# Optimization experiments

Measured on AMD Instinct MI355X. Metric: run time of the kernel, lower is better.

The kernel has to match this reference:

```python
import jax, jax.numpy as jnp
import numpy as np

NUM_HEADS = 16
D_IN = 1024
D_OUT = 64  # = D_IN // NUM_HEADS
N = 2048


def setup_inputs() -> dict:
    key = jax.random.key(0)
    kx, kq, kk, kv, ko = jax.random.split(key, 5)
    x = jax.random.normal(kx, (N, D_IN), dtype=jnp.float32)
    # per-head projection weights, stacked over heads (torch code keeps a
    # Python list of SelfAttention modules; stacking is the vectorized form)
    q_proj = jax.random.normal(kq, (NUM_HEADS, D_IN, D_OUT), dtype=jnp.float32)
    k_proj = jax.random.normal(kk, (NUM_HEADS, D_IN, D_OUT), dtype=jnp.float32)
    v_proj = jax.random.normal(kv, (NUM_HEADS, D_IN, D_OUT), dtype=jnp.float32)
    o_proj = jax.random.normal(ko, (D_IN, D_IN), dtype=jnp.float32)
    return {"x": x, "q_proj": q_proj, "k_proj": k_proj, "v_proj": v_proj, "o_proj": o_proj}


def reference(x, q_proj, k_proj, v_proj, o_proj):
    d_out = q_proj.shape[-1]
    # per-head projections: [H, N, E]
    q = jnp.einsum('nd,hde->hne', x, q_proj)
    k = jnp.einsum('nd,hde->hne', x, k_proj)
    v = jnp.einsum('nd,hde->hne', x, v_proj)
    # full NxN scores per head (matches the naive torch implementation's math)
    scores = jnp.einsum('hne,hme->hnm', q, k) / jnp.sqrt(jnp.float32(d_out))
    attn = jax.nn.softmax(scores, axis=-1)
    ctx = jnp.einsum('hnm,hme->hne', attn, v)
    # concat heads along the feature dim (head 0 first, as in torch.cat)
    h, n, e = ctx.shape
    out = jnp.transpose(ctx, (1, 0, 2)).reshape(n, h * e)
    return out @ o_proj
```

## Files before the change

kernel.cpp:

```cpp
#include <hip/hip_runtime.h>

#define H 16
#define N 2048
#define E 64
#define D 1024

typedef __attribute__((ext_vector_type(8))) short bf16x8;
typedef __attribute__((ext_vector_type(4))) float f32x4;
typedef __attribute__((ext_vector_type(4))) unsigned int u32x4;

__device__ __forceinline__ float bf2f(unsigned short u) {
    union { unsigned int i; float f; } v;
    v.i = ((unsigned int)u) << 16;
    return v.f;
}
__device__ __forceinline__ unsigned short f2bf(float f) {
    unsigned int u = __float_as_uint(f);
    return (unsigned short)((u + 0x7fffu + ((u >> 16) & 1u)) >> 16);
}
__device__ __forceinline__ unsigned int cvtpk(float lo, float hi) {
    unsigned int r;
    asm("v_cvt_pk_bf16_f32 %0, %1, %2" : "=v"(r) : "v"(lo), "v"(hi));
    return r;
}
__device__ __forceinline__ bf16x8 pk4(unsigned int a, unsigned int b,
                                      unsigned int c, unsigned int d) {
    union { u32x4 u; bf16x8 h; } x;
    x.u = (u32x4){a, b, c, d};
    return x.h;
}
#define MFMA(a, b, c) __builtin_amdgcn_mfma_f32_16x16x32_bf16(a, b, c, 0, 0, 0)

typedef __attribute__((address_space(3))) unsigned int lds_u32;
typedef const __attribute__((address_space(1))) unsigned int glb_u32;
__device__ __forceinline__ void dma16(const unsigned short* g, unsigned short* l) {
    __builtin_amdgcn_global_load_lds((glb_u32*)g, (lds_u32*)l, 16, 0, 0);
}

__device__ __forceinline__ int sw8(int row, int c)  { return row * 64  + ((c ^ (row & 7)) << 3); }

__global__ __launch_bounds__(256) void convert_all_kernel(
    const float* __restrict__ x,
    const float* __restrict__ qw, const float* __restrict__ kw,
    const float* __restrict__ vw, const float* __restrict__ ow,
    unsigned short* __restrict__ xh, unsigned short* __restrict__ xl,
    unsigned short* __restrict__ wBh, unsigned short* __restrict__ wBl,
    unsigned short* __restrict__ wvt, unsigned short* __restrict__ woh)
{
    __shared__ float ts[64][65];
    const int b0 = blockIdx.x;
    const int t = threadIdx.x;
    if (b0 < 2048) {
        const int i = (b0 * 256 + t) * 4;
        const float4 v = *(const float4*)&x[i];
        ushort4 hh, ll;
        hh.x = f2bf(v.x); ll.x = f2bf(v.x - bf2f(hh.x));
        hh.y = f2bf(v.y); ll.y = f2bf(v.y - bf2f(hh.y));
        hh.z = f2bf(v.z); ll.z = f2bf(v.z - bf2f(hh.z));
        hh.w = f2bf(v.w); ll.w = f2bf(v.w - bf2f(hh.w));
        *(ushort4*)&xh[i] = hh;
        *(ushort4*)&xl[i] = ll;
        return;
    }
    const int b = b0 - 2048;
    const float* src;
    int rs, dt, orow0;
    bool has_lo;
    unsigned short *dh, *dl;
    if (b < 768) {
        const int which = b >> 8, r = b & 255, h = r >> 4;
        dt = r & 15;
        src = (which == 0 ? qw : which == 1 ? kw : vw) + ((size_t)h * D + dt * 64) * E;
        rs = E;
        if (which == 0)      { dh = wBh; dl = wBl; orow0 = h * 64;        has_lo = true; }
        else if (which == 1) { dh = wBh; dl = wBl; orow0 = 1024 + h * 64; has_lo = true; }
        else                 { dh = wvt; dl = wBl; orow0 = h * 64;        has_lo = false; }
    } else {
        const int r = b - 768, ct = r >> 4;
        dt = r & 15;
        src = ow + (size_t)(dt * 64) * D + ct * 64;
        rs = D;
        orow0 = ct * 64;
        dh = woh; dl = wBl; has_lo = false;
    }
    {
        const int row = t >> 2, cb = (t & 3) * 16;
        #pragma unroll
        for (int j = 0; j < 16; j += 4) {
            const float4 v = *(const float4*)&src[row * rs + cb + j];
            ts[row][cb + j + 0] = v.x;
            ts[row][cb + j + 1] = v.y;
            ts[row][cb + j + 2] = v.z;
            ts[row][cb + j + 3] = v.w;
        }
    }
    __syncthreads();
    {
        const int cl = t >> 2, dp = (t & 3) * 16;
        bf16x8 hv0, hv1, lv0, lv1;
        #pragma unroll
        for (int i = 0; i < 16; ++i) {
            const float f = ts[dp + i][cl];
            const unsigned short hh = f2bf(f);
            const unsigned short lo = f2bf(f - bf2f(hh));
            if (i < 8) { hv0[i] = (short)hh; lv0[i] = (short)lo; }
            else       { hv1[i - 8] = (short)hh; lv1[i - 8] = (short)lo; }
        }
        const size_t o = (size_t)(orow0 + cl) * D + dt * 64 + dp;
        *(bf16x8*)&dh[o] = hv0;
        *(bf16x8*)&dh[o + 8] = hv1;
        if (has_lo) {
            *(bf16x8*)&dl[o] = lv0;
            *(bf16x8*)&dl[o + 8] = lv1;
        }
    }
}

__global__ __launch_bounds__(256, 3) void qkv_kernel(
    const unsigned short* __restrict__ xh, const unsigned short* __restrict__ xl,
    const unsigned short* __restrict__ wBh, const unsigned short* __restrict__ wBl,
    const unsigned short* __restrict__ wvt,
    unsigned short* __restrict__ Qh, unsigned short* __restrict__ Ql,
    unsigned short* __restrict__ Kh, unsigned short* __restrict__ Kl,
    unsigned short* __restrict__ Vt)
{
    __shared__ unsigned short ash[128 * 64], asl[128 * 64];
    __shared__ unsigned short bsh[64 * 64], bsl[64 * 64];
    const int n0 = blockIdx.x * 128;
    const int ct0 = blockIdx.y;
    const int sec = ct0 >> 4;
    const int hh = ct0 & 15;
    const bool isv = (sec == 2);
    const unsigned short* Bh = isv ? wvt : wBh;
    const size_t brow0 = (sec == 1 ? 1024 : 0) + hh * 64;

    const int t = threadIdx.x;
    const int lane = t & 63, wvi = t >> 6, quad = lane >> 4, l15 = lane & 15;

    f32x4 acc[2][4];
    #pragma unroll
    for (int i = 0; i < 2; ++i)
        #pragma unroll
        for (int j = 0; j < 4; ++j) acc[i][j] = (f32x4){0.f, 0.f, 0.f, 0.f};

    for (int k0 = 0; k0 < D; k0 += 64) {
        __syncthreads();
        #pragma unroll
        for (int p = 0; p < 4; ++p) {
            const int row = p * 32 + wvi * 8 + (lane >> 3);
            const int lc = (lane & 7) ^ (row & 7);
            const int lo = p * 2048 + wvi * 512 + lane * 8;
            const size_t ga = (size_t)(n0 + row) * D + k0 + lc * 8;
            dma16(&xh[ga], &ash[lo]);
            if (!isv) dma16(&xl[ga], &asl[lo]);
        }
        #pragma unroll
        for (int p = 0; p < 2; ++p) {
            const int row = p * 32 + wvi * 8 + (lane >> 3);
            const int lc = (lane & 7) ^ (row & 7);
            const int lo = p * 2048 + wvi * 512 + lane * 8;
            const size_t gb = (brow0 + row) * D + k0 + lc * 8;
            dma16(&Bh[gb], &bsh[lo]);
            if (!isv) dma16(&wBl[gb], &bsl[lo]);
        }
        __syncthreads();

        #pragma unroll
        for (int kwi = 0; kwi < 2; ++kwi) {
            const int c = kwi * 4 + quad;
            bf16x8 ah[2], al[2], bh[4], bl[4];
            #pragma unroll
            for (int i = 0; i < 2; ++i) {
                ah[i] = *(const bf16x8*)&ash[sw8(wvi * 32 + i * 16 + l15, c)];
                if (!isv) al[i] = *(const bf16x8*)&asl[sw8(wvi * 32 + i * 16 + l15, c)];
            }
            #pragma unroll
            for (int j = 0; j < 4; ++j) {
                bh[j] = *(const bf16x8*)&bsh[sw8(j * 16 + l15, c)];
                if (!isv) bl[j] = *(const bf16x8*)&bsl[sw8(j * 16 + l15, c)];
            }
            #pragma unroll
            for (int i = 0; i < 2; ++i)
                #pragma unroll
                for (int j = 0; j < 4; ++j) {
                    acc[i][j] = MFMA(ah[i], bh[j], acc[i][j]);
                    if (!isv) {
                        acc[i][j] = MFMA(ah[i], bl[j], acc[i][j]);
                        acc[i][j] = MFMA(al[i], bh[j], acc[i][j]);
                    }
                }
        }
    }

    if (isv) {
        #pragma unroll
        for (int j = 0; j < 4; ++j) {
            const int e = j * 16 + l15;
            #pragma unroll
            for (int i = 0; i < 2; ++i) {
                const int nb = n0 + wvi * 32 + i * 16 + quad * 4;
                ushort4 pk;
                pk.x = f2bf(acc[i][j][0]);
                pk.y = f2bf(acc[i][j][1]);
                pk.z = f2bf(acc[i][j][2]);
                pk.w = f2bf(acc[i][j][3]);
                *(ushort4*)&Vt[((size_t)hh * 64 + e) * N + nb] = pk;
            }
        }
    } else {
        const float scale = (sec == 0) ? 0.125f : 1.0f;
        unsigned short* Oh = (sec == 0) ? Qh : Kh;
        unsigned short* Ol = (sec == 0) ? Ql : Kl;
        #pragma unroll
        for (int j = 0; j < 4; ++j) {
            const int e = j * 16 + l15;
            #pragma unroll
            for (int i = 0; i < 2; ++i)
                #pragma unroll
                for (int r = 0; r < 4; ++r) {
                    const int n = n0 + wvi * 32 + i * 16 + quad * 4 + r;
                    const float val = acc[i][j][r] * scale;
                    const unsigned short hv = f2bf(val);
                    Oh[((size_t)hh * N + n) * E + e] = hv;
                    Ol[((size_t)hh * N + n) * E + e] = f2bf(val - bf2f(hv));
                }
        }
    }
}

__global__ __launch_bounds__(256, 2) void attn_kernel(
    const unsigned short* __restrict__ Qh, const unsigned short* __restrict__ Ql,
    const unsigned short* __restrict__ Kh, const unsigned short* __restrict__ Kl,
    const unsigned short* __restrict__ Vt,
    unsigned short* __restrict__ Op0, unsigned short* __restrict__ Op1,
    float* __restrict__ mlp)
{
    __shared__ unsigned short kbuf[2 * 16384];
    __shared__ unsigned short vts[64 * 128];
    const int r0 = blockIdx.x * 128, h = blockIdx.y, split = blockIdx.z;
    const int mb = split * 1024;
    const int t = threadIdx.x, lane = t & 63, wvi = t >> 6, quad = lane >> 4, l15 = lane & 15;

    bf16x8 qfh[2][2], qfl[2][2];
    #pragma unroll
    for (int i = 0; i < 2; ++i) {
        const size_t base = ((size_t)h * N + r0 + wvi * 32 + i * 16 + l15) * E;
        #pragma unroll
        for (int kwi = 0; kwi < 2; ++kwi) {
            qfh[i][kwi] = *(const bf16x8*)&Qh[base + kwi * 32 + quad * 8];
            qfl[i][kwi] = *(const bf16x8*)&Ql[base + kwi * 32 + quad * 8];
        }
    }

    f32x4 oacc[2][4];
    float mrow[2] = {-1e30f, -1e30f}, lrow[2] = {0.f, 0.f};
    #pragma unroll
    for (int i = 0; i < 2; ++i)
        #pragma unroll
        for (int j = 0; j < 4; ++j) oacc[i][j] = (f32x4){0.f, 0.f, 0.f, 0.f};

    const int ve = wvi * 16 + (lane >> 2);
    const int vc = lane & 3;

    #pragma unroll
    for (int p = 0; p < 4; ++p) {
        const int row = p * 32 + wvi * 8 + (lane >> 3);
        const int lc = (lane & 7) ^ (row & 7);
        const int lo = p * 2048 + wvi * 512 + lane * 8;
        const size_t gk = ((size_t)h * N + mb + row) * E + lc * 8;
        dma16(&Kh[gk], &kbuf[lo]);
        dma16(&Kl[gk], &kbuf[8192 + lo]);
    }

    for (int it = 0; it < 8; ++it) {
        const int cur = it & 1;
        __syncthreads();
        const int mcol = mb + it * 128;

        uint2 vr0[4], vr1[4];
        #pragma unroll
        for (int z = 0; z < 4; ++z) {
            const size_t gb = ((size_t)h * 64 + ve) * N + mcol + vc * 32 + z * 4;
            vr0[z] = *(const uint2*)&Vt[gb];
            vr1[z] = *(const uint2*)&Vt[gb + 16];
        }

        const unsigned short* ksh = &kbuf[cur * 16384];
        const unsigned short* ksl = ksh + 8192;

        f32x4 s[2][8];
        #pragma unroll
        for (int i = 0; i < 2; ++i)
            #pragma unroll
            for (int ct = 0; ct < 8; ++ct) s[i][ct] = (f32x4){0.f, 0.f, 0.f, 0.f};

        #pragma unroll
        for (int kwi = 0; kwi < 2; ++kwi) {
            const int c = kwi * 4 + quad;
            #pragma unroll
            for (int ct = 0; ct < 8; ++ct) {
                const bf16x8 kh = *(const bf16x8*)&ksh[sw8(ct * 16 + l15, c)];
                const bf16x8 kl = *(const bf16x8*)&ksl[sw8(ct * 16 + l15, c)];
                #pragma unroll
                for (int i = 0; i < 2; ++i) {
                    s[i][ct] = MFMA(kh, qfh[i][kwi], s[i][ct]);
                    s[i][ct] = MFMA(kl, qfh[i][kwi], s[i][ct]);
                    s[i][ct] = MFMA(kh, qfl[i][kwi], s[i][ct]);
                }
            }
        }

        #pragma unroll
        for (int i = 0; i < 2; ++i) {
            float m0 = s[i][0][0], m1 = s[i][0][1], m2 = s[i][0][2], m3 = s[i][0][3];
            #pragma unroll
            for (int ct = 1; ct < 8; ++ct) {
                m0 = fmaxf(m0, s[i][ct][0]); m1 = fmaxf(m1, s[i][ct][1]);
                m2 = fmaxf(m2, s[i][ct][2]); m3 = fmaxf(m3, s[i][ct][3]);
            }
            float mx = fmaxf(fmaxf(m0, m1), fmaxf(m2, m3));
            mx = fmaxf(mx, __shfl_xor(mx, 16));
            mx = fmaxf(mx, __shfl_xor(mx, 32));
            const float mn = fmaxf(mrow[i], mx);
            const float al = __expf(mrow[i] - mn);
            mrow[i] = mn;
            float s0 = 0.f, s1 = 0.f, s2 = 0.f, s3 = 0.f;
            #pragma unroll
            for (int ct = 0; ct < 8; ++ct) {
                const float p0 = __expf(s[i][ct][0] - mn);
                const float p1 = __expf(s[i][ct][1] - mn);
                const float p2 = __expf(s[i][ct][2] - mn);
                const float p3 = __expf(s[i][ct][3] - mn);
                s[i][ct][0] = p0; s[i][ct][1] = p1;
                s[i][ct][2] = p2; s[i][ct][3] = p3;
                s0 += p0; s1 += p1; s2 += p2; s3 += p3;
            }
            float sum = (s0 + s1) + (s2 + s3);
            sum += __shfl_xor(sum, 16);
            sum += __shfl_xor(sum, 32);
            lrow[i] = lrow[i] * al + sum;
            #pragma unroll
            for (int ct = 0; ct < 4; ++ct) {
                oacc[i][ct][0] *= al; oacc[i][ct][1] *= al;
                oacc[i][ct][2] *= al; oacc[i][ct][3] *= al;
            }
        }

        #pragma unroll
        for (int z = 0; z < 4; ++z) {
            const int c16 = vc * 4 + z;
            u32x4 w = (u32x4){vr0[z].x, vr0[z].y, vr1[z].x, vr1[z].y};
            *(u32x4*)&vts[ve * 128 + ((c16 ^ (ve & 7)) << 3)] = w;
        }
        __syncthreads();

        if (it < 7) {
            #pragma unroll
            for (int p = 0; p < 4; ++p) {
                const int row = p * 32 + wvi * 8 + (lane >> 3);
                const int lc = (lane & 7) ^ (row & 7);
                const int lo = (cur ^ 1) * 16384 + p * 2048 + wvi * 512 + lane * 8;
                const size_t gk = ((size_t)h * N + mcol + 128 + row) * E + lc * 8;
                dma16(&Kh[gk], &kbuf[lo]);
                dma16(&Kl[gk], &kbuf[8192 + lo]);
            }
        }

        #pragma unroll
        for (int kb = 0; kb < 4; ++kb) {
            bf16x8 pb[2];
            #pragma unroll
            for (int i = 0; i < 2; ++i)
                pb[i] = pk4(cvtpk(s[i][2 * kb][0],     s[i][2 * kb][1]),
                            cvtpk(s[i][2 * kb][2],     s[i][2 * kb][3]),
                            cvtpk(s[i][2 * kb + 1][0], s[i][2 * kb + 1][1]),
                            cvtpk(s[i][2 * kb + 1][2], s[i][2 * kb + 1][3]));
            #pragma unroll
            for (int ct = 0; ct < 4; ++ct) {
                const int re = ct * 16 + l15;
                const bf16x8 va =
                    *(const bf16x8*)&vts[re * 128 + (((kb * 4 + quad) ^ (re & 7)) << 3)];
                #pragma unroll
                for (int i = 0; i < 2; ++i)
                    oacc[i][ct] = MFMA(va, pb[i], oacc[i][ct]);
            }
        }
    }

    unsigned short* Opc = split ? Op1 : Op0;
    #pragma unroll
    for (int i = 0; i < 2; ++i) {
        const int n = r0 + wvi * 32 + i * 16 + l15;
        if (quad == 0) {
            mlp[(((size_t)split * 16 + h) * 2048 + n) * 2 + 0] = mrow[i];
            mlp[(((size_t)split * 16 + h) * 2048 + n) * 2 + 1] = lrow[i];
        }
        #pragma unroll
        for (int ct = 0; ct < 4; ++ct) {
            ushort4 pk;
            pk.x = f2bf(oacc[i][ct][0]);
            pk.y = f2bf(oacc[i][ct][1]);
            pk.z = f2bf(oacc[i][ct][2]);
            pk.w = f2bf(oacc[i][ct][3]);
            *(ushort4*)&Opc[((size_t)h * 2048 + n) * 64 + ct * 16 + quad * 4] = pk;
        }
    }
}

__global__ __launch_bounds__(256) void combine_kernel(
    const unsigned short* __restrict__ Op0, const unsigned short* __restrict__ Op1,
    const float* __restrict__ mlp, unsigned short* __restrict__ Ch)
{
    const int h = blockIdx.y;
    const int n = blockIdx.x * 64 + (threadIdx.x >> 2);
    const int e0 = (threadIdx.x & 3) * 16;
    const float m0 = mlp[((size_t)h * 2048 + n) * 2 + 0];
    const float l0 = mlp[((size_t)h * 2048 + n) * 2 + 1];
    const float m1 = mlp[((size_t)(16 + h) * 2048 + n) * 2 + 0];
    const float l1 = mlp[((size_t)(16 + h) * 2048 + n) * 2 + 1];
    const float M = fmaxf(m0, m1);
    const float a0 = __expf(m0 - M), a1 = __expf(m1 - M);
    const float inv = 1.f / (l0 * a0 + l1 * a1);
    const size_t ib = ((size_t)h * 2048 + n) * 64 + e0;
    const size_t ob = (size_t)n * D + h * 64 + e0;
    #pragma unroll
    for (int j = 0; j < 2; ++j) {
        const bf16x8 v0 = *(const bf16x8*)&Op0[ib + j * 8];
        const bf16x8 v1 = *(const bf16x8*)&Op1[ib + j * 8];
        bf16x8 o;
        #pragma unroll
        for (int k = 0; k < 8; ++k) {
            const float c = (bf2f((unsigned short)v0[k]) * a0 +
                             bf2f((unsigned short)v1[k]) * a1) * inv;
            o[k] = (short)f2bf(c);
        }
        *(bf16x8*)&Ch[ob + j * 8] = o;
    }
}

__global__ __launch_bounds__(256, 4) void out_proj_kernel(
    const unsigned short* __restrict__ Chh, const unsigned short* __restrict__ Wh,
    float* __restrict__ out)
{
    __shared__ unsigned short ash[64 * 64], bsh[64 * 64];
    const int n0 = blockIdx.x * 64, c0 = blockIdx.y * 64;
    const int t = threadIdx.x, lane = t & 63, wvi = t >> 6, quad = lane >> 4, l15 = lane & 15;

    f32x4 acc[4];
    #pragma unroll
    for (int j = 0; j < 4; ++j) acc[j] = (f32x4){0.f, 0.f, 0.f, 0.f};

    for (int k0 = 0; k0 < D; k0 += 64) {
        __syncthreads();
        #pragma unroll
        for (int p = 0; p < 2; ++p) {
            const int row = p * 32 + wvi * 8 + (lane >> 3);
            const int lc = (lane & 7) ^ (row & 7);
            const int lo = p * 2048 + wvi * 512 + lane * 8;
            dma16(&Chh[(size_t)(n0 + row) * D + k0 + lc * 8], &ash[lo]);
            dma16(&Wh[(size_t)(c0 + row) * D + k0 + lc * 8], &bsh[lo]);
        }
        __syncthreads();

        #pragma unroll
        for (int kwi = 0; kwi < 2; ++kwi) {
            const int c = kwi * 4 + quad;
            const bf16x8 ah = *(const bf16x8*)&ash[sw8(wvi * 16 + l15, c)];
            #pragma unroll
            for (int j = 0; j < 4; ++j) {
                const bf16x8 bh = *(const bf16x8*)&bsh[sw8(j * 16 + l15, c)];
                acc[j] = MFMA(ah, bh, acc[j]);
            }
        }
    }

    #pragma unroll
    for (int r = 0; r < 4; ++r) {
        const int n = n0 + wvi * 16 + quad * 4 + r;
        #pragma unroll
        for (int j = 0; j < 4; ++j)
            out[(size_t)n * D + c0 + j * 16 + l15] = acc[j][r];
    }
}

extern "C" void kernel_launch(void* const* d_in, const int* in_sizes, int n_in,
                              void* d_out, int out_size, void* d_ws, size_t ws_size,
                              hipStream_t stream) {
    const float* x  = (const float*)d_in[0];
    const float* qw = (const float*)d_in[1];
    const float* kw = (const float*)d_in[2];
    const float* vw = (const float*)d_in[3];
    const float* ow = (const float*)d_in[4];
    float* out = (float*)d_out;

    unsigned short* ws = (unsigned short*)d_ws;
    const size_t M1 = 1024 * 1024;
    unsigned short* wBh = ws;
    unsigned short* wBl = ws + 2 * M1;
    unsigned short* wvt = ws + 4 * M1;
    unsigned short* woh = ws + 5 * M1;
    unsigned short* xh  = ws + 6 * M1;
    unsigned short* xl  = ws + 8 * M1;
    unsigned short* Qh  = ws + 10 * M1;
    unsigned short* Ql  = ws + 12 * M1;
    unsigned short* Kh  = ws + 14 * M1;
    unsigned short* Kl  = ws + 16 * M1;
    unsigned short* Vt  = ws + 18 * M1;
    unsigned short* Ch  = xh;

    unsigned short* Op0 = wBh;
    unsigned short* Op1 = wBl;
    float* mlp = (float*)wvt;

    convert_all_kernel<<<3072, 256, 0, stream>>>(x, qw, kw, vw, ow,
                                                 xh, xl, wBh, wBl, wvt, woh);
    qkv_kernel<<<dim3(16, 48), 256, 0, stream>>>(xh, xl, wBh, wBl, wvt,
                                                 Qh, Ql, Kh, Kl, Vt);
    attn_kernel<<<dim3(16, 16, 2), 256, 0, stream>>>(Qh, Ql, Kh, Kl, Vt,
                                                     Op0, Op1, mlp);
    combine_kernel<<<dim3(32, 16), 256, 0, stream>>>(Op0, Op1, mlp, Ch);
    out_proj_kernel<<<dim3(32, 16), 256, 0, stream>>>(Ch, woh, out);
}
```

Baseline: 164.3 us.

## Enlarge Q/K projection tiles to 128x128 and raise MFMA priority in attention

```diff
diff --git a/kernel.cpp b/kernel.cpp
--- a/kernel.cpp
+++ b/kernel.cpp
@@ -116,7 +116,7 @@
     }
 }
 
-__global__ __launch_bounds__(256, 3) void qkv_kernel(
+__global__ __launch_bounds__(256, 2) void qkv_kernel(
     const unsigned short* __restrict__ xh, const unsigned short* __restrict__ xl,
     const unsigned short* __restrict__ wBh, const unsigned short* __restrict__ wBl,
     const unsigned short* __restrict__ wvt,
@@ -125,17 +125,86 @@
     unsigned short* __restrict__ Vt)
 {
     __shared__ unsigned short ash[128 * 64], asl[128 * 64];
-    __shared__ unsigned short bsh[64 * 64], bsl[64 * 64];
+    __shared__ unsigned short bsh[128 * 64], bsl[128 * 64];
     const int n0 = blockIdx.x * 128;
-    const int ct0 = blockIdx.y;
-    const int sec = ct0 >> 4;
-    const int hh = ct0 & 15;
-    const bool isv = (sec == 2);
-    const unsigned short* Bh = isv ? wvt : wBh;
-    const size_t brow0 = (sec == 1 ? 1024 : 0) + hh * 64;
-
+    const int y = blockIdx.y;
     const int t = threadIdx.x;
     const int lane = t & 63, wvi = t >> 6, quad = lane >> 4, l15 = lane & 15;
+
+    if (y < 16) {
+        const int sec = y >> 3;
+        const int col0 = (y & 7) * 128;
+        const size_t brow0 = (size_t)sec * 1024 + col0;
+        const int wr = wvi >> 1, wc = wvi & 1;
+
+        f32x4 acc[4][4];
+        #pragma unroll
+        for (int i = 0; i < 4; ++i)
+            #pragma unroll
+            for (int j = 0; j < 4; ++j) acc[i][j] = (f32x4){0.f, 0.f, 0.f, 0.f};
+
+        for (int k0 = 0; k0 < D; k0 += 64) {
+            __syncthreads();
+            #pragma unroll
+            for (int p = 0; p < 4; ++p) {
+                const int row = p * 32 + wvi * 8 + (lane >> 3);
+                const int lc = (lane & 7) ^ (row & 7);
+                const int lo = p * 2048 + wvi * 512 + lane * 8;
+                const size_t ga = (size_t)(n0 + row) * D + k0 + lc * 8;
+                dma16(&xh[ga], &ash[lo]);
+                dma16(&xl[ga], &asl[lo]);
+                const size_t gb = (brow0 + row) * D + k0 + lc * 8;
+                dma16(&wBh[gb], &bsh[lo]);
+                dma16(&wBl[gb], &bsl[lo]);
+            }
+            __syncthreads();
+
+            #pragma unroll
+            for (int kwi = 0; kwi < 2; ++kwi) {
+                const int c = kwi * 4 + quad;
+                bf16x8 bh[4], bl[4];
+                #pragma unroll
+                for (int j = 0; j < 4; ++j) {
+                    bh[j] = *(const bf16x8*)&bsh[sw8(wc * 64 + j * 16 + l15, c)];
+                    bl[j] = *(const bf16x8*)&bsl[sw8(wc * 64 + j * 16 + l15, c)];
+                }
+                #pragma unroll
+                for (int i = 0; i < 4; ++i) {
+                    const bf16x8 ah = *(const bf16x8*)&ash[sw8(wr * 64 + i * 16 + l15, c)];
+                    const bf16x8 al = *(const bf16x8*)&asl[sw8(wr * 64 + i * 16 + l15, c)];
+                    #pragma unroll
+                    for (int j = 0; j < 4; ++j) {
+                        acc[i][j] = MFMA(ah, bh[j], acc[i][j]);
+                        acc[i][j] = MFMA(ah, bl[j], acc[i][j]);
+                        acc[i][j] = MFMA(al, bh[j], acc[i][j]);
+                    }
+                }
+            }
+        }
+
+        const float scale = (sec == 0) ? 0.125f : 1.0f;
+        unsigned short* Oh = (sec == 0) ? Qh : Kh;
+        unsigned short* Ol = (sec == 0) ? Ql : Kl;
+        const int hbase = (y & 7) * 2 + (wvi & 1);
+        #pragma unroll
+        for (int j = 0; j < 4; ++j) {
+            const int e = j * 16 + l15;
+            #pragma unroll
+            for (int i = 0; i < 4; ++i)
+                #pragma unroll
+                for (int r = 0; r < 4; ++r) {
+                    const int n = n0 + wr * 64 + i * 16 + quad * 4 + r;
+                    const float val = acc[i][j][r] * scale;
+                    const unsigned short hv = f2bf(val);
+                    Oh[((size_t)hbase * N + n) * E + e] = hv;
+                    Ol[((size_t)hbase * N + n) * E + e] = f2bf(val - bf2f(hv));
+                }
+        }
+        return;
+    }
+
+    const int hh = y - 16;
+    const size_t brow0 = (size_t)hh * 64;
 
     f32x4 acc[2][4];
     #pragma unroll
@@ -150,80 +219,46 @@
             const int row = p * 32 + wvi * 8 + (lane >> 3);
             const int lc = (lane & 7) ^ (row & 7);
             const int lo = p * 2048 + wvi * 512 + lane * 8;
-            const size_t ga = (size_t)(n0 + row) * D + k0 + lc * 8;
-            dma16(&xh[ga], &ash[lo]);
-            if (!isv) dma16(&xl[ga], &asl[lo]);
+            dma16(&xh[(size_t)(n0 + row) * D + k0 + lc * 8], &ash[lo]);
         }
         #pragma unroll
         for (int p = 0; p < 2; ++p) {
             const int row = p * 32 + wvi * 8 + (lane >> 3);
             const int lc = (lane & 7) ^ (row & 7);
             const int lo = p * 2048 + wvi * 512 + lane * 8;
-            const size_t gb = (brow0 + row) * D + k0 + lc * 8;
-            dma16(&Bh[gb], &bsh[lo]);
-            if (!isv) dma16(&wBl[gb], &bsl[lo]);
+            dma16(&wvt[(brow0 + row) * D + k0 + lc * 8], &bsh[lo]);
         }
         __syncthreads();
 
         #pragma unroll
         for (int kwi = 0; kwi < 2; ++kwi) {
             const int c = kwi * 4 + quad;
-            bf16x8 ah[2], al[2], bh[4], bl[4];
+            bf16x8 bh[4];
+            #pragma unroll
+            for (int j = 0; j < 4; ++j)
+                bh[j] = *(const bf16x8*)&bsh[sw8(j * 16 + l15, c)];
             #pragma unroll
             for (int i = 0; i < 2; ++i) {
-                ah[i] = *(const bf16x8*)&ash[sw8(wvi * 32 + i * 16 + l15, c)];
-                if (!isv) al[i] = *(const bf16x8*)&asl[sw8(wvi * 32 + i * 16 + l15, c)];
-            }
-            #pragma unroll
-            for (int j = 0; j < 4; ++j) {
-                bh[j] = *(const bf16x8*)&bsh[sw8(j * 16 + l15, c)];
-                if (!isv) bl[j] = *(const bf16x8*)&bsl[sw8(j * 16 + l15, c)];
-            }
-            #pragma unroll
-            for (int i = 0; i < 2; ++i)
+                const bf16x8 ah = *(const bf16x8*)&ash[sw8(wvi * 32 + i * 16 + l15, c)];
                 #pragma unroll
-                for (int j = 0; j < 4; ++j) {
-                    acc[i][j] = MFMA(ah[i], bh[j], acc[i][j]);
-                    if (!isv) {
-                        acc[i][j] = MFMA(ah[i], bl[j], acc[i][j]);
-                        acc[i][j] = MFMA(al[i], bh[j], acc[i][j]);
-                    }
-                }
-        }
-    }
-
-    if (isv) {
-        #pragma unroll
-        for (int j = 0; j < 4; ++j) {
-            const int e = j * 16 + l15;
-            #pragma unroll
-            for (int i = 0; i < 2; ++i) {
-                const int nb = n0 + wvi * 32 + i * 16 + quad * 4;
-                ushort4 pk;
-                pk.x = f2bf(acc[i][j][0]);
-                pk.y = f2bf(acc[i][j][1]);
-                pk.z = f2bf(acc[i][j][2]);
-                pk.w = f2bf(acc[i][j][3]);
-                *(ushort4*)&Vt[((size_t)hh * 64 + e) * N + nb] = pk;
-            }
-        }
-    } else {
-        const float scale = (sec == 0) ? 0.125f : 1.0f;
-        unsigned short* Oh = (sec == 0) ? Qh : Kh;
-        unsigned short* Ol = (sec == 0) ? Ql : Kl;
-        #pragma unroll
-        for (int j = 0; j < 4; ++j) {
-            const int e = j * 16 + l15;
-            #pragma unroll
-            for (int i = 0; i < 2; ++i)
-                #pragma unroll
-                for (int r = 0; r < 4; ++r) {
-                    const int n = n0 + wvi * 32 + i * 16 + quad * 4 + r;
-                    const float val = acc[i][j][r] * scale;
-                    const unsigned short hv = f2bf(val);
-                    Oh[((size_t)hh * N + n) * E + e] = hv;
-                    Ol[((size_t)hh * N + n) * E + e] = f2bf(val - bf2f(hv));
-                }
+                for (int j = 0; j < 4; ++j)
+                    acc[i][j] = MFMA(ah, bh[j], acc[i][j]);
+            }
+        }
+    }
+
+    #pragma unroll
+    for (int j = 0; j < 4; ++j) {
+        const int e = j * 16 + l15;
+        #pragma unroll
+        for (int i = 0; i < 2; ++i) {
+            const int nb = n0 + wvi * 32 + i * 16 + quad * 4;
+            ushort4 pk;
+            pk.x = f2bf(acc[i][j][0]);
+            pk.y = f2bf(acc[i][j][1]);
+            pk.z = f2bf(acc[i][j][2]);
+            pk.w = f2bf(acc[i][j][3]);
+            *(ushort4*)&Vt[((size_t)hh * 64 + e) * N + nb] = pk;
         }
     }
 }
@@ -294,6 +329,7 @@
             #pragma unroll
             for (int ct = 0; ct < 8; ++ct) s[i][ct] = (f32x4){0.f, 0.f, 0.f, 0.f};
 
+        __builtin_amdgcn_s_setprio(1);
         #pragma unroll
         for (int kwi = 0; kwi < 2; ++kwi) {
             const int c = kwi * 4 + quad;
@@ -309,6 +345,7 @@
                 }
             }
         }
+        __builtin_amdgcn_s_setprio(0);
 
         #pragma unroll
         for (int i = 0; i < 2; ++i) {
@@ -375,6 +412,7 @@
                             cvtpk(s[i][2 * kb][2],     s[i][2 * kb][3]),
                             cvtpk(s[i][2 * kb + 1][0], s[i][2 * kb + 1][1]),
                             cvtpk(s[i][2 * kb + 1][2], s[i][2 * kb + 1][3]));
+            __builtin_amdgcn_s_setprio(1);
             #pragma unroll
             for (int ct = 0; ct < 4; ++ct) {
                 const int re = ct * 16 + l15;
@@ -384,6 +422,7 @@
                 for (int i = 0; i < 2; ++i)
                     oacc[i][ct] = MFMA(va, pb[i], oacc[i][ct]);
             }
+            __builtin_amdgcn_s_setprio(0);
         }
     }
 
@@ -514,7 +553,7 @@
 
     convert_all_kernel<<<3072, 256, 0, stream>>>(x, qw, kw, vw, ow,
                                                  xh, xl, wBh, wBl, wvt, woh);
-    qkv_kernel<<<dim3(16, 48), 256, 0, stream>>>(xh, xl, wBh, wBl, wvt,
+    qkv_kernel<<<dim3(16, 32), 256, 0, stream>>>(xh, xl, wBh, wBl, wvt,
                                                  Qh, Ql, Kh, Kl, Vt);
     attn_kernel<<<dim3(16, 16, 2), 256, 0, stream>>>(Qh, Ql, Kh, Kl, Vt,
                                                      Op0, Op1, mlp);
```

After: 167.2 us. No clear change (+1.7%).

## Fuse split-KV combine into out-projection, skip redundant rescale, add MFMA priority

Applied to the files above, without the earlier changes.

```diff
diff --git a/kernel.cpp b/kernel.cpp
--- a/kernel.cpp
+++ b/kernel.cpp
@@ -294,6 +294,7 @@
             #pragma unroll
             for (int ct = 0; ct < 8; ++ct) s[i][ct] = (f32x4){0.f, 0.f, 0.f, 0.f};
 
+        __builtin_amdgcn_s_setprio(1);
         #pragma unroll
         for (int kwi = 0; kwi < 2; ++kwi) {
             const int c = kwi * 4 + quad;
@@ -309,6 +310,7 @@
                 }
             }
         }
+        __builtin_amdgcn_s_setprio(0);
 
         #pragma unroll
         for (int i = 0; i < 2; ++i) {
@@ -321,9 +323,18 @@
             float mx = fmaxf(fmaxf(m0, m1), fmaxf(m2, m3));
             mx = fmaxf(mx, __shfl_xor(mx, 16));
             mx = fmaxf(mx, __shfl_xor(mx, 32));
-            const float mn = fmaxf(mrow[i], mx);
-            const float al = __expf(mrow[i] - mn);
-            mrow[i] = mn;
+            if (__any(mx > mrow[i])) {
+                const float mn = fmaxf(mrow[i], mx);
+                const float al = __expf(mrow[i] - mn);
+                mrow[i] = mn;
+                lrow[i] *= al;
+                #pragma unroll
+                for (int ct = 0; ct < 4; ++ct) {
+                    oacc[i][ct][0] *= al; oacc[i][ct][1] *= al;
+                    oacc[i][ct][2] *= al; oacc[i][ct][3] *= al;
+                }
+            }
+            const float mn = mrow[i];
             float s0 = 0.f, s1 = 0.f, s2 = 0.f, s3 = 0.f;
             #pragma unroll
             for (int ct = 0; ct < 8; ++ct) {
@@ -338,12 +349,7 @@
             float sum = (s0 + s1) + (s2 + s3);
             sum += __shfl_xor(sum, 16);
             sum += __shfl_xor(sum, 32);
-            lrow[i] = lrow[i] * al + sum;
-            #pragma unroll
-            for (int ct = 0; ct < 4; ++ct) {
-                oacc[i][ct][0] *= al; oacc[i][ct][1] *= al;
-                oacc[i][ct][2] *= al; oacc[i][ct][3] *= al;
-            }
+            lrow[i] += sum;
         }
 
         #pragma unroll
@@ -375,6 +381,7 @@
                             cvtpk(s[i][2 * kb][2],     s[i][2 * kb][3]),
                             cvtpk(s[i][2 * kb + 1][0], s[i][2 * kb + 1][1]),
                             cvtpk(s[i][2 * kb + 1][2], s[i][2 * kb + 1][3]));
+            __builtin_amdgcn_s_setprio(1);
             #pragma unroll
             for (int ct = 0; ct < 4; ++ct) {
                 const int re = ct * 16 + l15;
@@ -384,6 +391,7 @@
                 for (int i = 0; i < 2; ++i)
                     oacc[i][ct] = MFMA(va, pb[i], oacc[i][ct]);
             }
+            __builtin_amdgcn_s_setprio(0);
         }
     }
 
@@ -407,39 +415,9 @@
     }
 }
 
-__global__ __launch_bounds__(256) void combine_kernel(
+__global__ __launch_bounds__(256, 4) void out_proj_kernel(
     const unsigned short* __restrict__ Op0, const unsigned short* __restrict__ Op1,
-    const float* __restrict__ mlp, unsigned short* __restrict__ Ch)
-{
-    const int h = blockIdx.y;
-    const int n = blockIdx.x * 64 + (threadIdx.x >> 2);
-    const int e0 = (threadIdx.x & 3) * 16;
-    const float m0 = mlp[((size_t)h * 2048 + n) * 2 + 0];
-    const float l0 = mlp[((size_t)h * 2048 + n) * 2 + 1];
-    const float m1 = mlp[((size_t)(16 + h) * 2048 + n) * 2 + 0];
-    const float l1 = mlp[((size_t)(16 + h) * 2048 + n) * 2 + 1];
-    const float M = fmaxf(m0, m1);
-    const float a0 = __expf(m0 - M), a1 = __expf(m1 - M);
-    const float inv = 1.f / (l0 * a0 + l1 * a1);
-    const size_t ib = ((size_t)h * 2048 + n) * 64 + e0;
-    const size_t ob = (size_t)n * D + h * 64 + e0;
-    #pragma unroll
-    for (int j = 0; j < 2; ++j) {
-        const bf16x8 v0 = *(const bf16x8*)&Op0[ib + j * 8];
-        const bf16x8 v1 = *(const bf16x8*)&Op1[ib + j * 8];
-        bf16x8 o;
-        #pragma unroll
-        for (int k = 0; k < 8; ++k) {
-            const float c = (bf2f((unsigned short)v0[k]) * a0 +
-                             bf2f((unsigned short)v1[k]) * a1) * inv;
-            o[k] = (short)f2bf(c);
-        }
-        *(bf16x8*)&Ch[ob + j * 8] = o;
-    }
-}
-
-__global__ __launch_bounds__(256, 4) void out_proj_kernel(
-    const unsigned short* __restrict__ Chh, const unsigned short* __restrict__ Wh,
+    const float* __restrict__ mlp, const unsigned short* __restrict__ Wh,
     float* __restrict__ out)
 {
     __shared__ unsigned short ash[64 * 64], bsh[64 * 64];
@@ -451,14 +429,38 @@
     for (int j = 0; j < 4; ++j) acc[j] = (f32x4){0.f, 0.f, 0.f, 0.f};
 
     for (int k0 = 0; k0 < D; k0 += 64) {
+        const int hp = k0 >> 6;
         __syncthreads();
         #pragma unroll
         for (int p = 0; p < 2; ++p) {
             const int row = p * 32 + wvi * 8 + (lane >> 3);
             const int lc = (lane & 7) ^ (row & 7);
             const int lo = p * 2048 + wvi * 512 + lane * 8;
-            dma16(&Chh[(size_t)(n0 + row) * D + k0 + lc * 8], &ash[lo]);
             dma16(&Wh[(size_t)(c0 + row) * D + k0 + lc * 8], &bsh[lo]);
+        }
+        #pragma unroll
+        for (int p = 0; p < 2; ++p) {
+            const int row = p * 32 + wvi * 8 + (lane >> 3);
+            const int lc = (lane & 7) ^ (row & 7);
+            const int n = n0 + row;
+            const float m0 = mlp[((size_t)hp * 2048 + n) * 2 + 0];
+            const float l0 = mlp[((size_t)hp * 2048 + n) * 2 + 1];
+            const float m1 = mlp[((size_t)(16 + hp) * 2048 + n) * 2 + 0];
+            const float l1 = mlp[((size_t)(16 + hp) * 2048 + n) * 2 + 1];
+            const float M = fmaxf(m0, m1);
+            float a0 = __expf(m0 - M), a1 = __expf(m1 - M);
+            const float inv = 1.f / (l0 * a0 + l1 * a1);
+            a0 *= inv; a1 *= inv;
+            const size_t ib = ((size_t)hp * 2048 + n) * 64 + lc * 8;
+            const bf16x8 v0 = *(const bf16x8*)&Op0[ib];
+            const bf16x8 v1 = *(const bf16x8*)&Op1[ib];
+            bf16x8 o;
+            #pragma unroll
+            for (int k = 0; k < 8; ++k)
+                o[k] = (short)f2bf(bf2f((unsigned short)v0[k]) * a0 +
+                                   bf2f((unsigned short)v1[k]) * a1);
+            const int lo = p * 2048 + wvi * 512 + lane * 8;
+            *(bf16x8*)&ash[lo] = o;
         }
         __syncthreads();
 
@@ -506,7 +508,6 @@
     unsigned short* Kh  = ws + 14 * M1;
     unsigned short* Kl  = ws + 16 * M1;
     unsigned short* Vt  = ws + 18 * M1;
-    unsigned short* Ch  = xh;
 
     unsigned short* Op0 = wBh;
     unsigned short* Op1 = wBl;
@@ -518,6 +519,5 @@
                                                  Qh, Ql, Kh, Kl, Vt);
     attn_kernel<<<dim3(16, 16, 2), 256, 0, stream>>>(Qh, Ql, Kh, Kl, Vt,
                                                      Op0, Op1, mlp);
-    combine_kernel<<<dim3(32, 16), 256, 0, stream>>>(Op0, Op1, mlp, Ch);
-    out_proj_kernel<<<dim3(32, 16), 256, 0, stream>>>(Ch, woh, out);
-}
+    out_proj_kernel<<<dim3(32, 16), 256, 0, stream>>>(Op0, Op1, mlp, woh, out);
+}
```

New measurement: 168.9 us. 2.8% more time.
